# Optimization experiments

Measured on AMD Instinct MI355X. Metric: run time of the kernel, lower is better.

## Reference

```python
import jax, jax.numpy as jnp
import numpy as np

NQ, NC, D = 100000, 2000, 128
QN, CN, MAXC = 4, 4, 4
B, S = 128, 64
HOPS, RANK_K = 2, 10


def setup_inputs() -> dict:
    key = jax.random.key(0)
    ks = jax.random.split(key, 24)
    sc = 1.0 / np.sqrt(D)
    f = lambda k, shape: (jax.random.normal(k, shape) * sc).astype(jnp.float32)
    xb = float(np.sqrt(6.0 / (B + D)))  # xavier_uniform on [B, D]
    return {
        'embed_question': f(ks[0], (NQ, D)),
        'embed_concept': f(ks[1], (NC, D)),
        'embed_correctness': f(ks[2], (2, D)),
        'W_ih1': f(ks[3], (3 * D, 2 * D)), 'W_hh1': f(ks[4], (3 * D, D)),
        'b_ih1': jnp.zeros(3 * D), 'b_hh1': jnp.zeros(3 * D),
        'W_ih2': f(ks[5], (3 * D, D)), 'W_hh2': f(ks[6], (3 * D, D)),
        'b_ih2': jnp.zeros(3 * D), 'b_hh2': jnp.zeros(3 * D),
        'W_agg': f(ks[7], (HOPS, D, D)), 'b_agg': jnp.zeros((HOPS, D)),
        'W_last': f(ks[8], (D, D)), 'b_last': jnp.zeros(D),
        'W_query': f(ks[9], (D, D)), 'b_query': jnp.zeros(D),
        'W_key': f(ks[10], (D, D)), 'b_key': jnp.zeros(D),
        'w_q': f(ks[11], (D,)), 'w_k': f(ks[12], (D,)), 'b_w': jnp.zeros(()),
        'h1_init': jax.random.uniform(ks[13], (B, D), minval=-xb, maxval=xb),
        'h2_init': jax.random.uniform(ks[14], (B, D), minval=-xb, maxval=xb),
        'question_neighbors': jax.random.randint(ks[15], (NQ, QN), 0, NC),
        'concept_neighbors': jax.random.randint(ks[16], (NC, CN), 0, NQ),
        'q2c': jax.random.randint(ks[17], (NQ, MAXC), 0, NC),
        'question_seq': jax.random.randint(ks[18], (B, S), 0, NQ),
        'correctness_seq': jax.random.randint(ks[19], (B, S), 0, 2),
        'mask_seq': jax.random.randint(ks[20], (B, S), 0, 2),
    }


def _gru(x, h, Wih, Whh, bih, bhh):
    gi = x @ Wih.T + bih
    gh = h @ Whh.T + bhh
    ir, iz, inn = jnp.split(gi, 3, axis=-1)
    hr, hz, hn = jnp.split(gh, 3, axis=-1)
    r = jax.nn.sigmoid(ir + hr)
    z = jax.nn.sigmoid(iz + hz)
    n = jnp.tanh(inn + r * hn)
    return (1.0 - z) * n + z * h


def _aggregate(embs, W_agg, b_agg, W_last, b_last):
    embs = list(embs)
    for i in range(HOPS):
        for j in range(HOPS - i):
            m = jnp.mean(embs[j + 1], axis=-2) + embs[j]
            embs[j] = jnp.tanh(m @ W_agg[j].T + b_agg[j])
    return jnp.tanh(embs[0] @ W_last.T + b_last)


def _predict(qc, states, W_query, b_query, W_key, b_key, w_q, w_k, b_w):
    # qc: [B, nqc, D]; states: [B, nst, D]
    og = jnp.einsum('bqd,bsd->bqs', qc, states)
    Qe = jnp.tanh(qc @ W_key.T + b_key)          # MLP_key(question_concepts)
    Ke = jnp.tanh(states @ W_query.T + b_query)  # MLP_query(states)
    tmp = (Qe @ w_q)[:, :, None] + (Ke @ w_k)[:, None, :] + b_w  # [B,nqc,nst]
    alpha = jax.nn.softmax(tmp, axis=2)
    return jax.nn.sigmoid(jnp.sum(alpha * og, axis=(1, 2)))


def reference(embed_question, embed_concept, embed_correctness,
              W_ih1, W_hh1, b_ih1, b_hh1, W_ih2, W_hh2, b_ih2, b_hh2,
              W_agg, b_agg, W_last, b_last, W_query, b_query, W_key, b_key,
              w_q, w_k, b_w, h1_init, h2_init,
              question_neighbors, concept_neighbors, q2c,
              question_seq, correctness_seq, mask_seq):
    h1, h2 = h1_init, h2_init
    state_history = jnp.zeros((B, S, D), jnp.float32)
    y = jnp.zeros((B, S), jnp.float32)
    for t in range(S - 1):
        q_t = question_seq[:, t]
        mask_t = mask_seq[:, t] != 0
        emb_r = embed_correctness[correctness_seq[:, t]]
        # multi-hop neighbor expansion (computed for full batch; masked rows
        # are replaced below, identical math to the original masked gather)
        nodes = [q_t]
        for i in range(HOPS):
            flat = nodes[-1].reshape(-1)
            tbl = question_neighbors if i % 2 == 0 else concept_neighbors
            nxt = tbl[flat]
            nodes.append(nxt.reshape(nodes[-1].shape + (nxt.shape[-1],)))
        embs = [embed_question[n] if i % 2 == 0 else embed_concept[n]
                for i, n in enumerate(nodes)]
        agg = _aggregate(embs, W_agg, b_agg, W_last, b_last)
        emb_q = jnp.where(mask_t[:, None], agg, embed_question[q_t])
        h1 = _gru(jnp.concatenate([emb_q, emb_r], axis=1), h1, W_ih1, W_hh1, b_ih1, b_hh1)
        g2 = _gru(h1, h2, W_ih2, W_hh2, b_ih2, b_hh2)
        q_next = question_seq[:, t + 1]
        qc = jnp.concatenate([embed_question[q_next][:, None],
                              embed_concept[q2c[q_next]]], axis=1)  # [B, 1+MAXC, D]
        if t == 0:
            y = y.at[:, 0].set(_predict(qc, g2[:, None], W_query, b_query, W_key, b_key, w_q, w_k, b_w))
            continue  # original skips h2/state_history update at t==0
        cur = g2[:, None]
        if t <= RANK_K:
            hist = jnp.concatenate([cur, state_history[:, :t]], axis=1)
        else:
            Qv = jax.lax.stop_gradient(embed_question[q_next])               # [B,D]
            Kv = jax.lax.stop_gradient(embed_question[question_seq[:, :t]])  # [B,t,D]
            scores = jnp.einsum('btd,bd->bt', Kv, Qv)
            _, idx = jax.lax.top_k(scores, RANK_K)
            sel = jnp.take_along_axis(state_history, idx[:, :, None], axis=1)
            hist = jnp.concatenate([cur, sel], axis=1)
        y = y.at[:, t + 1].set(_predict(qc, hist, W_query, b_query, W_key, b_key, w_q, w_k, b_w))
        h2 = g2
        state_history = state_history.at[:, t].set(g2)
    return y
```

## Files before the change

kernel.cpp:

```cpp
#include <hip/hip_runtime.h>
#include <math.h>

#define D    128
#define QN   4
#define CN   4
#define MAXC 4
#define BB   128
#define SS   64
#define RK   10
#define T    768

#define UOFF_IH1A 0
#define UOFF_IH1B 24576
#define UOFF_HH1  49152
#define UOFF_IH2  73728
#define UOFF_HH2  98304
#define UOFF_QRY  122880
#define UOFF_A0   131072
#define UOFF_A1   139264
#define UOFF_LS   147456
#define TOTAL_U   155648

typedef _Float16 h2_t __attribute__((ext_vector_type(2)));
union U32H2 { unsigned u; h2_t h; unsigned short s2[2]; };

__device__ __forceinline__ unsigned h16f(float x){
  U32H2 c; c.h[0] = (_Float16)x; c.h[1] = (_Float16)0.f;
  return (unsigned)c.s2[0];
}
__device__ __forceinline__ unsigned packh2(float a, float b){
  U32H2 c; c.h[0] = (_Float16)a; c.h[1] = (_Float16)b;
  return c.u;
}
__device__ __forceinline__ float dot2(unsigned w, unsigned x, float acc){
  U32H2 a; a.u = w; U32H2 b; b.u = x;
  return __builtin_amdgcn_fdot2(a.h, b.h, acc, false);
}
__device__ __forceinline__ float hlo(unsigned u){ U32H2 a; a.u=u; return (float)a.h[0]; }
__device__ __forceinline__ float hhi(unsigned u){ U32H2 a; a.u=u; return (float)a.h[1]; }

__device__ __forceinline__ float fsig(float x){ return 1.f/(1.f + __expf(-x)); }
__device__ __forceinline__ float ftanh(float x){
  float xc = fminf(fmaxf(x, -30.f), 30.f);
  float e = __expf(2.f*xc);
  return (e - 1.f)/(e + 1.f);
}

#define FD4(w4, x4, acc) { \
  acc = dot2((w4).x, (x4).x, acc); acc = dot2((w4).y, (x4).y, acc); \
  acc = dot2((w4).z, (x4).z, acc); acc = dot2((w4).w, (x4).w, acc); }

__global__ void gikt_pack(const float* __restrict__ Wih1,
                          const float* __restrict__ Whh1,
                          const float* __restrict__ Wih2,
                          const float* __restrict__ Whh2,
                          const float* __restrict__ Wagg,
                          const float* __restrict__ Wlast,
                          const float* __restrict__ Wqry,
                          unsigned* __restrict__ wsU)
{
  int i = blockIdx.x * blockDim.x + threadIdx.x;
  if (i >= TOTAL_U) return;
  const float* src = nullptr; int row = 0, e2 = 0, stride = 0;
  int j = i;
  if (j < 24576) {
    int c = j & 3, i4 = j >> 2, k = i4 / 768, t = i4 - k * 768, r = t >> 1, hf = t & 1;
    e2 = hf * 32 + k * 4 + c; row = r; src = Wih1; stride = 256;
  } else if ((j -= 24576) < 24576) {
    e2 = 64 + (j / 384); row = j % 384; src = Wih1; stride = 256;
  } else if ((j -= 24576) < 24576) {
    int c = j & 3, i4 = j >> 2, k = i4 / 768, t = i4 - k * 768, r = t >> 1, hf = t & 1;
    e2 = hf * 32 + k * 4 + c; row = r; src = Whh1; stride = 128;
  } else if ((j -= 24576) < 24576) {
    int c = j & 3, i4 = j >> 2, k = i4 / 768, t = i4 - k * 768, r = t >> 1, hf = t & 1;
    e2 = hf * 32 + k * 4 + c; row = r; src = Wih2; stride = 128;
  } else if ((j -= 24576) < 24576) {
    int c = j & 3, i4 = j >> 2, k = i4 / 768, t = i4 - k * 768, r = t >> 1, hf = t & 1;
    e2 = hf * 32 + k * 4 + c; row = r; src = Whh2; stride = 128;
  } else if ((j -= 24576) < 8192) {
    int c = j & 3, i4 = j >> 2, k = i4 >> 7, r = i4 & 127;
    e2 = k * 4 + c; row = r; src = Wqry; stride = 128;
  } else if ((j -= 8192) < 8192) {
    int r = j & 127, p = (j >> 7) & 1, e2g = j >> 8;
    e2 = 2 * e2g + p; row = r; src = Wagg; stride = 128;
  } else if ((j -= 8192) < 8192) {
    int r = j & 127, p = (j >> 7) & 1, e2g = j >> 8;
    e2 = 2 * e2g + p; row = r; src = Wagg + 128 * 128; stride = 128;
  } else {
    j -= 8192;
    int r = j & 127, p = (j >> 7) & 1, e2g = j >> 8;
    e2 = 2 * e2g + p; row = r; src = Wlast; stride = 128;
  }
  float lo = src[row * stride + 2 * e2];
  float hi = src[row * stride + 2 * e2 + 1];
  wsU[i] = h16f(lo) | (h16f(hi) << 16);
}

__device__ __forceinline__ float2 gru_nl2(float2 gr, float2 gz, float2 gn,
                                          float2 hr, float2 hz, float2 hn,
                                          float2 hold){
  float2 out;
  {
    float rg = fsig(gr.x + hr.x);
    float zg = fsig(gz.x + hz.x);
    float ng = ftanh(gn.x + rg*hn.x);
    out.x = (1.f-zg)*ng + zg*hold.x;
  }
  {
    float rg = fsig(gr.y + hr.y);
    float zg = fsig(gz.y + hz.y);
    float ng = ftanh(gn.y + rg*hn.y);
    out.y = (1.f-zg)*ng + zg*hold.y;
  }
  return out;
}

__launch_bounds__(T, 1)
__global__ void gikt_main(
    const float* __restrict__ embQ,
    const float* __restrict__ embC,
    const float* __restrict__ embR,
    const float* __restrict__ b_ih1,
    const float* __restrict__ b_hh1,
    const float* __restrict__ b_ih2,
    const float* __restrict__ b_hh2,
    const float* __restrict__ b_agg,
    const float* __restrict__ b_last,
    const float* __restrict__ b_query,
    const float* __restrict__ w_k,
    const float* __restrict__ h1i,
    const float* __restrict__ h2i,
    const int* __restrict__ qnbr,
    const int* __restrict__ cnbr,
    const int* __restrict__ q2c,
    const int* __restrict__ qseq,
    const int* __restrict__ cseq,
    const int* __restrict__ mseq,
    const unsigned* __restrict__ wsU,
    float* __restrict__ y)
{
  const int b   = blockIdx.x;
  const int tid = threadIdx.x;
  const int r2  = tid >> 1, hf = tid & 1;

  __shared__ unsigned aggL[3 * 8192];
  __shared__ __align__(16) float hist[SS][132];
  __shared__ float gicorr[2][384];
  __shared__ int   idxk[SS][RK];
  __shared__ float kwh[SS];
  __shared__ __align__(16) float a_[5][D];
  __shared__ __align__(16) float gi1[3*D];
  __shared__ __align__(16) float gh1[3*D];
  __shared__ __align__(16) float gi2[3*D];
  __shared__ __align__(16) float gh2[3*D];
  __shared__ __align__(16) float h1fp[2][D];
  __shared__ __align__(16) float g2fp[2][D];
  __shared__ __align__(16) float h2ifp[D];
  __shared__ float e0[D];
  __shared__ __align__(16) float qcs[2][D];
  __shared__ float kevec[D];
  __shared__ __align__(16) unsigned mPu[5][64];
  __shared__ __align__(16) unsigned vPu[64];
  __shared__ __align__(16) unsigned m1Pu[64];
  __shared__ __align__(16) unsigned xvPu[64];
  __shared__ __align__(16) unsigned h1Pu[64];
  __shared__ __align__(16) unsigned g2Pu[64];
  __shared__ __align__(16) unsigned h2iPu[64];
  __shared__ int   sq[SS], scc[SS], smk[SS];
  __shared__ int   nn1[SS][QN], nn2[SS][QN*CN], cc2[SS][MAXC];
  __shared__ float red[12];
  __shared__ float ogv[16], kwv[16];

  float (*G)[65] = (float(*)[65])aggL;

  uint4 pw1i[8], pw1h[8], pwi[8], pwh[8];
  {
    const uint4* Pa = (const uint4*)(wsU + UOFF_IH1A);
    const uint4* Pb = (const uint4*)(wsU + UOFF_HH1);
    const uint4* Pi = (const uint4*)(wsU + UOFF_IH2);
    const uint4* Ph = (const uint4*)(wsU + UOFF_HH2);
    #pragma unroll
    for (int k = 0; k < 8; ++k) {
      pw1i[k] = Pa[k*768 + tid]; pw1h[k] = Pb[k*768 + tid];
      pwi[k]  = Pi[k*768 + tid]; pwh[k]  = Ph[k*768 + tid];
    }
  }

  for (int i = tid; i < SS; i += T) { sq[i]=qseq[b*SS+i]; scc[i]=cseq[b*SS+i]; smk[i]=mseq[b*SS+i]; }
  __syncthreads();

  for (int i = tid; i < SS*32; i += T) {
    int s = i >> 5, e4 = i & 31;
    float4 v = ((const float4*)(embQ + sq[s]*D))[e4];
    ((float4*)hist[s])[e4] = v;
  }
  for (int i = tid; i < (SS-1)*QN; i += T)   { int t = i>>2, j = i&3; nn1[t][j] = qnbr[sq[t]*QN + j]; }
  for (int i = tid; i < (SS-1)*MAXC; i += T) { int t = i>>2, j = i&3; cc2[t][j] = q2c[sq[t+1]*MAXC + j]; }
  __syncthreads();

  for (int p = tid; p < SS*SS; p += T) {
    int tq = p >> 6, s = p & 63;
    if (tq >= RK+2 && s < tq-1) {
      const float4* ra = (const float4*)hist[tq];
      const float4* rb = (const float4*)hist[s];
      float acc = 0.f;
      #pragma unroll 8
      for (int d4 = 0; d4 < 32; ++d4) {
        float4 xa = ra[d4], xb = rb[d4];
        acc += xa.x*xb.x + xa.y*xb.y + xa.z*xb.z + xa.w*xb.w;
      }
      G[tq-(RK+2)][s] = acc;
    }
  }
  for (int i = tid; i < (SS-1)*QN*CN; i += T) {
    int t = i>>4, j = (i>>2)&3, l = i&3;
    nn2[t][j*CN+l] = cnbr[nn1[t][j]*CN + l];
  }
  {
    const int c = (tid >= 384) ? 1 : 0, r = tid - (c ? 384 : 0);
    const float2* er2 = (const float2*)(embR + c*D);
    float acc = 0.f;
    #pragma unroll 4
    for (int e2l = 0; e2l < 64; ++e2l) {
      unsigned u = wsU[UOFF_IH1B + e2l*384 + r];
      float2 x = er2[e2l];
      acc += hlo(u)*x.x + hhi(u)*x.y;
    }
    gicorr[c][r] = acc;
  }
  __syncthreads();

  if (tid < 52) {
    int t = RK + 1 + tid;
    for (int k = 0; k < RK; ++k) {
      float best = -INFINITY; int bi = 0;
      for (int s = 0; s < t; ++s) { float v = G[tid][s]; if (v > best) { best = v; bi = s; } }
      idxk[t][k] = bi;
      G[tid][bi] = -INFINITY;
    }
  }
  __syncthreads();

  for (int i = tid; i < 3*8192; i += T) aggL[i] = wsU[UOFF_A0 + i];
  if (tid < 64) {
    float a0 = h1i[b*D+2*tid], a1 = h1i[b*D+2*tid+1];
    h1Pu[tid] = packh2(a0, a1);
    ((float2*)h1fp[1])[tid] = make_float2(a0, a1);
    float c0 = h2i[b*D+2*tid], c1 = h2i[b*D+2*tid+1];
    h2iPu[tid] = packh2(c0, c1);
    ((float2*)h2ifp)[tid] = make_float2(c0, c1);
    g2Pu[tid] = 0;
  }
  if (tid < D) hist[0][tid] = 0.f;
  if (tid == 0) y[b*SS + 1] = 0.f;
  {
    float p0 = (tid < D) ? w_k[tid]*ftanh(b_query[tid]) : 0.f;
    #pragma unroll
    for (int off = 32; off; off >>= 1) p0 += __shfl_down(p0, off);
    if ((tid & 63) == 0) red[tid >> 6] = p0;
  }
  __syncthreads();
  if (tid == 0) kwh[0] = red[0]+red[1];
  __syncthreads();

  const uint4* Wq4 = (const uint4*)(wsU + UOFF_QRY);

  for (int t = 0; t < SS-1; ++t) {
    const int tp = t - 1;
    const bool msk = (smk[t] != 0);

    if (tid < 64 && t >= 1) {
      const int l = tid;
      const float* ph2 = (t <= 2) ? h2ifp : g2fp[t & 1];
      float2 hold = ((const float2*)ph2)[l];
      float2 gv = gru_nl2(((const float2*)gi2)[l], ((const float2*)(gi2+128))[l], ((const float2*)(gi2+256))[l],
                          ((const float2*)gh2)[l], ((const float2*)(gh2+128))[l], ((const float2*)(gh2+256))[l],
                          hold);
      ((float2*)g2fp[(t+1)&1])[l] = gv;
      g2Pu[l] = packh2(gv.x, gv.y);
      if (t >= 2) { hist[t-1][2*l] = gv.x; hist[t-1][2*l+1] = gv.y; }
    }
    if (msk) {
      const int d   = tid & 127;
      const int grp = tid >> 7;
      if (grp == 0) {
        float ev = embQ[sq[t]*D + d];
        float s1 = embC[nn1[t][0]*D+d]+embC[nn1[t][1]*D+d]+embC[nn1[t][2]*D+d]+embC[nn1[t][3]*D+d];
        ((_Float16*)mPu[0])[d] = (_Float16)(ev + 0.25f*s1);
      } else if (grp <= 4) {
        const int j = grp - 1;
        float e1v = embC[nn1[t][j]*D + d];
        float s2  = embQ[nn2[t][j*CN+0]*D+d]+embQ[nn2[t][j*CN+1]*D+d]
                   +embQ[nn2[t][j*CN+2]*D+d]+embQ[nn2[t][j*CN+3]*D+d];
        ((_Float16*)mPu[grp])[d] = (_Float16)(e1v + 0.25f*s2);
      } else {
        float acc = embQ[sq[t+1]*D + d];
        #pragma unroll
        for (int mm = 0; mm < MAXC; ++mm) acc += embC[cc2[t][mm]*D + d];
        qcs[t & 1][d] = acc;
      }
    } else {
      const int d   = tid & 127;
      const int grp = tid >> 7;
      if (grp == 0) {
        ((_Float16*)xvPu)[d] = (_Float16)(embQ[sq[t]*D + d]);
      } else if (grp == 5) {
        float acc = embQ[sq[t+1]*D + d];
        #pragma unroll
        for (int mm = 0; mm < MAXC; ++mm) acc += embC[cc2[t][mm]*D + d];
        qcs[t & 1][d] = acc;
      }
    }
    __syncthreads();

    if (msk) {
      if (tid < 128) {
        const int r = tid;
        const unsigned* A = aggL;
        const uint2* x2p = (const uint2*)mPu[0];
        float acc0 = b_agg[r], acc1 = 0.f;
        #pragma unroll
        for (int e2g = 0; e2g < 32; e2g += 2) {
          unsigned u00 = A[e2g*256 + r],     u01 = A[e2g*256 + 128 + r];
          uint2 x0 = x2p[e2g];
          acc0 = dot2(u00, x0.x, acc0); acc0 = dot2(u01, x0.y, acc0);
          unsigned u10 = A[(e2g+1)*256 + r], u11 = A[(e2g+1)*256 + 128 + r];
          uint2 x1 = x2p[e2g+1];
          acc1 = dot2(u10, x1.x, acc1); acc1 = dot2(u11, x1.y, acc1);
        }
        a_[0][r] = ftanh(acc0 + acc1);
      } else if (tid < 256) {
        const int r = tid - 128;
        const unsigned* A = aggL + 8192;
        const uint2* x1p = (const uint2*)mPu[1];
        const uint2* x2p = (const uint2*)mPu[2];
        const uint2* x3p = (const uint2*)mPu[3];
        const uint2* x4p = (const uint2*)mPu[4];
        float bb = b_agg[D + r];
        float c1 = 0.f, c2 = 0.f, c3 = 0.f, c4 = 0.f;
        #pragma unroll
        for (int e2g = 0; e2g < 32; ++e2g) {
          unsigned u0 = A[e2g*256 + r], u1 = A[e2g*256 + 128 + r];
          uint2 v1 = x1p[e2g]; c1 = dot2(u0, v1.x, c1); c1 = dot2(u1, v1.y, c1);
          uint2 v2 = x2p[e2g]; c2 = dot2(u0, v2.x, c2); c2 = dot2(u1, v2.y, c2);
          uint2 v3 = x3p[e2g]; c3 = dot2(u0, v3.x, c3); c3 = dot2(u1, v3.y, c3);
          uint2 v4 = x4p[e2g]; c4 = dot2(u0, v4.x, c4); c4 = dot2(u1, v4.y, c4);
        }
        a_[1][r] = ftanh(bb + c1); a_[2][r] = ftanh(bb + c2);
        a_[3][r] = ftanh(bb + c3); a_[4][r] = ftanh(bb + c4);
      } else if (tid < 432 && t >= 1) {
        const int g = (tid - 256) >> 4, lane = tid & 15;
        const int ne = (tp < RK ? tp : RK) + 1;
        if (g < ne) {
          const float* row;
          if (g == 0) row = g2fp[(t+1)&1];
          else {
            int s = (tp <= RK) ? (g-1) : idxk[tp][g-1];
            row = hist[s];
            if (lane == 0) kwv[g] = kwh[s];
          }
          const float* qp = qcs[tp & 1];
          float part = 0.f;
          #pragma unroll
          for (int k = 0; k < 8; ++k) { int d = lane + (k<<4); part += qp[d]*row[d]; }
          part += __shfl_xor(part, 8, 16);
          part += __shfl_xor(part, 4, 16);
          part += __shfl_xor(part, 2, 16);
          part += __shfl_xor(part, 1, 16);
          if (lane == 0) ogv[g] = part;
        }
      } else if (tid >= 512) {
        const int rq = (tid - 512) >> 1, hq = tid & 1;
        const uint4* g2p4 = (const uint4*)g2Pu;
        float a0 = hq ? 0.f : b_query[rq], a1 = 0.f;
        #pragma unroll
        for (int k = hq*8; k < hq*8+8; k += 2) {
          uint4 u0 = Wq4[k*128 + rq];     uint4 x0 = g2p4[k];   FD4(u0, x0, a0);
          uint4 u1 = Wq4[(k+1)*128 + rq]; uint4 x1 = g2p4[k+1]; FD4(u1, x1, a1);
        }
        float acc = a0 + a1; acc += __shfl_xor(acc, 1);
        if (!hq) kevec[rq] = ftanh(acc) * w_k[rq];
      }
      __syncthreads();

      if (tid < 256) {
        const int l = tid & 63;
        float v0 = a_[0][2*l]   + 0.25f*(a_[1][2*l]  +a_[2][2*l]  +a_[3][2*l]  +a_[4][2*l]);
        float v1 = a_[0][2*l+1] + 0.25f*(a_[1][2*l+1]+a_[2][2*l+1]+a_[3][2*l+1]+a_[4][2*l+1]);
        vPu[l] = packh2(v0, v1);
        const int r = tid >> 1, h = tid & 1;
        const uint2* x2p = (const uint2*)vPu;
        float acc0 = h ? 0.f : b_agg[r], acc1 = 0.f;
        #pragma unroll
        for (int e2g = h*16; e2g < h*16+16; e2g += 2) {
          unsigned u00 = aggL[e2g*256 + r],     u01 = aggL[e2g*256 + 128 + r];
          uint2 x0 = x2p[e2g];
          acc0 = dot2(u00, x0.x, acc0); acc0 = dot2(u01, x0.y, acc0);
          unsigned u10 = aggL[(e2g+1)*256 + r], u11 = aggL[(e2g+1)*256 + 128 + r];
          uint2 x1 = x2p[e2g+1];
          acc1 = dot2(u10, x1.x, acc1); acc1 = dot2(u11, x1.y, acc1);
        }
        float acc = acc0 + acc1; acc += __shfl_xor(acc, 1);
        if (!h) ((_Float16*)m1Pu)[r] = (_Float16)ftanh(acc);
      } else if (tid >= 512 && tid < 576 && t >= 1) {
        const int lane = tid & 63;
        float v = kevec[lane] + kevec[lane + 64];
        #pragma unroll
        for (int off = 32; off; off >>= 1) v += __shfl_down(v, off);
        if (lane == 0) { kwv[0] = v; if (tp >= 1) kwh[tp] = v; }
      }
      __syncthreads();

      if (tid < 256) {
        const int r = tid >> 1, h = tid & 1;
        const unsigned* A = aggL + 16384;
        const uint2* x2p = (const uint2*)m1Pu;
        float acc0 = h ? 0.f : b_last[r], acc1 = 0.f;
        #pragma unroll
        for (int e2g = h*16; e2g < h*16+16; e2g += 2) {
          unsigned u00 = A[e2g*256 + r],     u01 = A[e2g*256 + 128 + r];
          uint2 x0 = x2p[e2g];
          acc0 = dot2(u00, x0.x, acc0); acc0 = dot2(u01, x0.y, acc0);
          unsigned u10 = A[(e2g+1)*256 + r], u11 = A[(e2g+1)*256 + 128 + r];
          uint2 x1 = x2p[e2g+1];
          acc1 = dot2(u10, x1.x, acc1); acc1 = dot2(u11, x1.y, acc1);
        }
        float acc = acc0 + acc1; acc += __shfl_xor(acc, 1);
        if (!h) ((_Float16*)xvPu)[r] = (_Float16)ftanh(acc);
      } else if (tid == 256 && t >= 1) {
        const int ne = (tp < RK ? tp : RK) + 1;
        float mx = kwv[0];
        for (int i2 = 1; i2 < ne; ++i2) mx = fmaxf(mx, kwv[i2]);
        float den = 0.f, num = 0.f;
        for (int i2 = 0; i2 < ne; ++i2) { float e_ = __expf(kwv[i2]-mx); den += e_; num += e_*ogv[i2]; }
        y[b*SS + ((tp==0) ? 0 : (tp+1))] = fsig(num/den);
      }
      __syncthreads();

      {
        const uint4* xvp4 = (const uint4*)xvPu;
        const uint4* h1p4 = (const uint4*)h1Pu;
        float ai0 = hf ? 0.f : (b_ih1[r2] + gicorr[scc[t]][r2]), ai1 = 0.f;
        float ah0 = hf ? 0.f : b_hh1[r2], ah1 = 0.f;
        #pragma unroll
        for (int k = 0; k < 8; k += 2) {
          uint4 xa = xvp4[hf*8+k], xb = xvp4[hf*8+k+1];
          FD4(pw1i[k], xa, ai0); FD4(pw1i[k+1], xb, ai1);
          uint4 ya = h1p4[hf*8+k], yb = h1p4[hf*8+k+1];
          FD4(pw1h[k], ya, ah0); FD4(pw1h[k+1], yb, ah1);
        }
        float acc_i = ai0 + ai1; acc_i += __shfl_xor(acc_i, 1);
        float acc_h = ah0 + ah1; acc_h += __shfl_xor(acc_h, 1);
        if (!hf) { gi1[r2] = acc_i; gh1[r2] = acc_h; }
      }
      __syncthreads();
    } else {
      if (tid >= 256 && tid < 432 && t >= 1) {
        const int g = (tid - 256) >> 4, lane = tid & 15;
        const int ne = (tp < RK ? tp : RK) + 1;
        if (g < ne) {
          const float* row;
          if (g == 0) row = g2fp[(t+1)&1];
          else {
            int s = (tp <= RK) ? (g-1) : idxk[tp][g-1];
            row = hist[s];
            if (lane == 0) kwv[g] = kwh[s];
          }
          const float* qp = qcs[tp & 1];
          float part = 0.f;
          #pragma unroll
          for (int k = 0; k < 8; ++k) { int d = lane + (k<<4); part += qp[d]*row[d]; }
          part += __shfl_xor(part, 8, 16);
          part += __shfl_xor(part, 4, 16);
          part += __shfl_xor(part, 2, 16);
          part += __shfl_xor(part, 1, 16);
          if (lane == 0) ogv[g] = part;
        }
      } else if (tid >= 512) {
        const int rq = (tid - 512) >> 1, hq = tid & 1;
        const uint4* g2p4 = (const uint4*)g2Pu;
        float a0 = hq ? 0.f : b_query[rq], a1 = 0.f;
        #pragma unroll
        for (int k = hq*8; k < hq*8+8; k += 2) {
          uint4 u0 = Wq4[k*128 + rq];     uint4 x0 = g2p4[k];   FD4(u0, x0, a0);
          uint4 u1 = Wq4[(k+1)*128 + rq]; uint4 x1 = g2p4[k+1]; FD4(u1, x1, a1);
        }
        float acc = a0 + a1; acc += __shfl_xor(acc, 1);
        if (!hq) kevec[rq] = ftanh(acc) * w_k[rq];
      }
      {
        const uint4* xvp4 = (const uint4*)xvPu;
        const uint4* h1p4 = (const uint4*)h1Pu;
        float ai0 = hf ? 0.f : (b_ih1[r2] + gicorr[scc[t]][r2]), ai1 = 0.f;
        float ah0 = hf ? 0.f : b_hh1[r2], ah1 = 0.f;
        #pragma unroll
        for (int k = 0; k < 8; k += 2) {
          uint4 xa = xvp4[hf*8+k], xb = xvp4[hf*8+k+1];
          FD4(pw1i[k], xa, ai0); FD4(pw1i[k+1], xb, ai1);
          uint4 ya = h1p4[hf*8+k], yb = h1p4[hf*8+k+1];
          FD4(pw1h[k], ya, ah0); FD4(pw1h[k+1], yb, ah1);
        }
        float acc_i = ai0 + ai1; acc_i += __shfl_xor(acc_i, 1);
        float acc_h = ah0 + ah1; acc_h += __shfl_xor(acc_h, 1);
        if (!hf) { gi1[r2] = acc_i; gh1[r2] = acc_h; }
      }
      __syncthreads();
    }

    if (!msk && t >= 1 && tid < 64) {
      float v = kevec[tid] + kevec[tid + 64];
      #pragma unroll
      for (int off = 32; off; off >>= 1) v += __shfl_down(v, off);
      if (tid == 0) {
        if (tp >= 1) kwh[tp] = v;
        const int ne = (tp < RK ? tp : RK) + 1;
        float mx = v;
        for (int i2 = 1; i2 < ne; ++i2) mx = fmaxf(mx, kwv[i2]);
        float den = __expf(v - mx), num = den*ogv[0];
        for (int i2 = 1; i2 < ne; ++i2) { float e_ = __expf(kwv[i2]-mx); den += e_; num += e_*ogv[i2]; }
        y[b*SS + ((tp==0) ? 0 : (tp+1))] = fsig(num/den);
      }
    }
    {
      const int l = tid & 63;
      float2 hold = ((const float2*)h1fp[(t+1)&1])[l];
      float2 hn = gru_nl2(((const float2*)gi1)[l], ((const float2*)(gi1+128))[l], ((const float2*)(gi1+256))[l],
                          ((const float2*)gh1)[l], ((const float2*)(gh1+128))[l], ((const float2*)(gh1+256))[l],
                          hold);
      ((float2*)h1fp[t&1])[l] = hn;
      h1Pu[l] = packh2(hn.x, hn.y);
    }
    {
      const uint4* xh1 = (const uint4*)h1Pu;
      const uint4* xh2 = (t <= 1) ? (const uint4*)h2iPu : (const uint4*)g2Pu;
      float ai0 = hf ? 0.f : b_ih2[r2], ai1 = 0.f;
      float ah0 = hf ? 0.f : b_hh2[r2], ah1 = 0.f;
      #pragma unroll
      for (int k = 0; k < 8; k += 2) {
        uint4 xa = xh1[hf*8+k], xb = xh1[hf*8+k+1];
        FD4(pwi[k], xa, ai0); FD4(pwi[k+1], xb, ai1);
        uint4 ya = xh2[hf*8+k], yb = xh2[hf*8+k+1];
        FD4(pwh[k], ya, ah0); FD4(pwh[k+1], yb, ah1);
      }
      float acc_i = ai0 + ai1; acc_i += __shfl_xor(acc_i, 1);
      float acc_h = ah0 + ah1; acc_h += __shfl_xor(acc_h, 1);
      if (!hf) { gi2[r2] = acc_i; gh2[r2] = acc_h; }
    }
    __syncthreads();
  }

  if (tid < 64) {
    const int l = tid;
    const float* ph2 = g2fp[1];
    float2 hold = ((const float2*)ph2)[l];
    float2 gv = gru_nl2(((const float2*)gi2)[l], ((const float2*)(gi2+128))[l], ((const float2*)(gi2+256))[l],
                        ((const float2*)gh2)[l], ((const float2*)(gh2+128))[l], ((const float2*)(gh2+256))[l],
                        hold);
    ((float2*)g2fp[0])[l] = gv;
    g2Pu[l] = packh2(gv.x, gv.y);
  }
  __syncthreads();
  if (tid < 128) {
    const int r = tid;
    const uint4* g2p4 = (const uint4*)g2Pu;
    float a0 = b_query[r], a1 = 0.f;
    #pragma unroll
    for (int k = 0; k < 16; k += 2) {
      uint4 u0 = Wq4[k*128 + r];     uint4 x0 = g2p4[k];   FD4(u0, x0, a0);
      uint4 u1 = Wq4[(k+1)*128 + r]; uint4 x1 = g2p4[k+1]; FD4(u1, x1, a1);
    }
    kevec[r] = ftanh(a0 + a1) * w_k[r];
  }
  __syncthreads();
  {
    const int tp = SS - 2;
    if (tid < 176) {
      const int g = tid >> 4, lane = tid & 15;
      const int ne = RK + 1;
      if (g < ne) {
        const float* row;
        if (g == 0) row = g2fp[0];
        else {
          int s = idxk[tp][g-1];
          row = hist[s];
          if (lane == 0) kwv[g] = kwh[s];
        }
        const float* qp = qcs[tp & 1];
        float part = 0.f;
        #pragma unroll
        for (int k = 0; k < 8; ++k) { int d = lane + (k<<4); part += qp[d]*row[d]; }
        part += __shfl_xor(part, 8, 16);
        part += __shfl_xor(part, 4, 16);
        part += __shfl_xor(part, 2, 16);
        part += __shfl_xor(part, 1, 16);
        if (lane == 0) ogv[g] = part;
      }
    } else if (tid >= 256 && tid < 320) {
      const int lane = tid & 63;
      float v = kevec[lane] + kevec[lane + 64];
      #pragma unroll
      for (int off = 32; off; off >>= 1) v += __shfl_down(v, off);
      if (lane == 0) kwv[0] = v;
    }
  }
  __syncthreads();
  if (tid == 0) {
    const int ne = RK + 1;
    float mx = kwv[0];
    for (int i2 = 1; i2 < ne; ++i2) mx = fmaxf(mx, kwv[i2]);
    float den = 0.f, num = 0.f;
    for (int i2 = 0; i2 < ne; ++i2) { float e_ = __expf(kwv[i2]-mx); den += e_; num += e_*ogv[i2]; }
    y[b*SS + SS - 1] = fsig(num/den);
  }
}

extern "C" void kernel_launch(void* const* d_in, const int* in_sizes, int n_in,
                              void* d_out, int out_size, void* d_ws, size_t ws_size,
                              hipStream_t stream)
{
  (void)in_sizes; (void)n_in; (void)out_size; (void)ws_size;

  const float* embQ  = (const float*)d_in[0];
  const float* embC  = (const float*)d_in[1];
  const float* embR  = (const float*)d_in[2];
  const float* Wih1  = (const float*)d_in[3];
  const float* Whh1  = (const float*)d_in[4];
  const float* bih1  = (const float*)d_in[5];
  const float* bhh1  = (const float*)d_in[6];
  const float* Wih2  = (const float*)d_in[7];
  const float* Whh2  = (const float*)d_in[8];
  const float* bih2  = (const float*)d_in[9];
  const float* bhh2  = (const float*)d_in[10];
  const float* Wagg  = (const float*)d_in[11];
  const float* bagg  = (const float*)d_in[12];
  const float* Wlast = (const float*)d_in[13];
  const float* blast = (const float*)d_in[14];
  const float* Wqry  = (const float*)d_in[15];
  const float* bqry  = (const float*)d_in[16];
  const float* wk    = (const float*)d_in[20];
  const float* h1i   = (const float*)d_in[22];
  const float* h2i   = (const float*)d_in[23];
  const int* qnbr    = (const int*)d_in[24];
  const int* cnbr    = (const int*)d_in[25];
  const int* q2c     = (const int*)d_in[26];
  const int* qseq    = (const int*)d_in[27];
  const int* cseq    = (const int*)d_in[28];
  const int* mseq    = (const int*)d_in[29];

  unsigned* wsU = (unsigned*)d_ws;
  float* yout = (float*)d_out;

  gikt_pack<<<(TOTAL_U + 255) / 256, 256, 0, stream>>>(Wih1, Whh1, Wih2, Whh2, Wagg, Wlast, Wqry, wsU);
  gikt_main<<<BB, T, 0, stream>>>(embQ, embC, embR, bih1, bhh1, bih2, bhh2, bagg, blast, bqry,
                                  wk, h1i, h2i, qnbr, cnbr, q2c, qseq, cseq, mseq, wsU, yout);
}
```

Before: 640.4 us.

## Prefetch next-step embedding gathers into registers and stream GRU1 weights from memory

The embedding and neighbour gathers for step t+1 are now issued into registers during step t, so their global-memory latency overlaps the barrier and the compute phases instead of sitting on the serial critical path. To make room for these registers, the layer-1 GRU weights are no longer held in registers; they are reloaded from the packed global buffer (likely L2-resident) on every step. An empty asm keeps the layer-2 weights pinned in registers. The trade-off is more per-step weight load traffic and latency in the GRU1 matvec in exchange for hidden gather latency and lower register pressure.

```diff
diff --git a/kernel.cpp b/kernel.cpp
--- a/kernel.cpp
+++ b/kernel.cpp
@@ -49,6 +49,8 @@
 #define FD4(w4, x4, acc) { \
   acc = dot2((w4).x, (x4).x, acc); acc = dot2((w4).y, (x4).y, acc); \
   acc = dot2((w4).z, (x4).z, acc); acc = dot2((w4).w, (x4).w, acc); }
+
+#define KEEP4(v) asm volatile("" : "+v"((v).x), "+v"((v).y), "+v"((v).z), "+v"((v).w))
 
 __global__ void gikt_pack(const float* __restrict__ Wih1,
                           const float* __restrict__ Whh1,
@@ -156,7 +158,6 @@
   __shared__ __align__(16) float h1fp[2][D];
   __shared__ __align__(16) float g2fp[2][D];
   __shared__ __align__(16) float h2ifp[D];
-  __shared__ float e0[D];
   __shared__ __align__(16) float qcs[2][D];
   __shared__ float kevec[D];
   __shared__ __align__(16) unsigned mPu[5][64];
@@ -173,17 +174,14 @@
 
   float (*G)[65] = (float(*)[65])aggL;
 
-  uint4 pw1i[8], pw1h[8], pwi[8], pwh[8];
+  uint4 pwi[8], pwh[8];
   {
-    const uint4* Pa = (const uint4*)(wsU + UOFF_IH1A);
-    const uint4* Pb = (const uint4*)(wsU + UOFF_HH1);
     const uint4* Pi = (const uint4*)(wsU + UOFF_IH2);
     const uint4* Ph = (const uint4*)(wsU + UOFF_HH2);
     #pragma unroll
-    for (int k = 0; k < 8; ++k) {
-      pw1i[k] = Pa[k*768 + tid]; pw1h[k] = Pb[k*768 + tid];
-      pwi[k]  = Pi[k*768 + tid]; pwh[k]  = Ph[k*768 + tid];
-    }
+    for (int k = 0; k < 8; ++k) { pwi[k] = Pi[k*768 + tid]; pwh[k] = Ph[k*768 + tid]; }
+    #pragma unroll
+    for (int k = 0; k < 8; ++k) { KEEP4(pwi[k]); KEEP4(pwh[k]); }
   }
 
   for (int i = tid; i < SS; i += T) { sq[i]=qseq[b*SS+i]; scc[i]=cseq[b*SS+i]; smk[i]=mseq[b*SS+i]; }
@@ -263,7 +261,31 @@
   if (tid == 0) kwh[0] = red[0]+red[1];
   __syncthreads();
 
+  const uint4* Wi1 = (const uint4*)(wsU + UOFF_IH1A);
+  const uint4* Wh1 = (const uint4*)(wsU + UOFF_HH1);
   const uint4* Wq4 = (const uint4*)(wsU + UOFF_QRY);
+
+  float pf0 = 0.f, pf1 = 0.f, pf2 = 0.f, pf3 = 0.f, pf4 = 0.f;
+
+#define PREFETCH(tt) {                                                        \
+    const int d_ = tid & 127, grp_ = tid >> 7;                                \
+    const bool m2_ = (smk[tt] != 0);                                          \
+    if (grp_ == 0) {                                                          \
+      pf0 = embQ[sq[tt]*D + d_];                                              \
+      if (m2_) { pf1 = embC[nn1[tt][0]*D+d_]; pf2 = embC[nn1[tt][1]*D+d_];    \
+                 pf3 = embC[nn1[tt][2]*D+d_]; pf4 = embC[nn1[tt][3]*D+d_]; }  \
+    } else if (grp_ <= 4) {                                                   \
+      if (m2_) { const int j_ = grp_ - 1;                                     \
+        pf0 = embC[nn1[tt][j_]*D + d_];                                       \
+        pf1 = embQ[nn2[tt][j_*CN+0]*D+d_]; pf2 = embQ[nn2[tt][j_*CN+1]*D+d_]; \
+        pf3 = embQ[nn2[tt][j_*CN+2]*D+d_]; pf4 = embQ[nn2[tt][j_*CN+3]*D+d_];}\
+    } else {                                                                  \
+      pf0 = embQ[sq[(tt)+1]*D + d_];                                          \
+      pf1 = embC[cc2[tt][0]*D+d_]; pf2 = embC[cc2[tt][1]*D+d_];               \
+      pf3 = embC[cc2[tt][2]*D+d_]; pf4 = embC[cc2[tt][3]*D+d_];               \
+    } }
+
+  PREFETCH(0);
 
   for (int t = 0; t < SS-1; ++t) {
     const int tp = t - 1;
@@ -280,37 +302,17 @@
       g2Pu[l] = packh2(gv.x, gv.y);
       if (t >= 2) { hist[t-1][2*l] = gv.x; hist[t-1][2*l+1] = gv.y; }
     }
-    if (msk) {
-      const int d   = tid & 127;
-      const int grp = tid >> 7;
-      if (grp == 0) {
-        float ev = embQ[sq[t]*D + d];
-        float s1 = embC[nn1[t][0]*D+d]+embC[nn1[t][1]*D+d]+embC[nn1[t][2]*D+d]+embC[nn1[t][3]*D+d];
-        ((_Float16*)mPu[0])[d] = (_Float16)(ev + 0.25f*s1);
-      } else if (grp <= 4) {
-        const int j = grp - 1;
-        float e1v = embC[nn1[t][j]*D + d];
-        float s2  = embQ[nn2[t][j*CN+0]*D+d]+embQ[nn2[t][j*CN+1]*D+d]
-                   +embQ[nn2[t][j*CN+2]*D+d]+embQ[nn2[t][j*CN+3]*D+d];
-        ((_Float16*)mPu[grp])[d] = (_Float16)(e1v + 0.25f*s2);
+    {
+      const int d = tid & 127, grp = tid >> 7;
+      if (msk) {
+        if (grp <= 4) ((_Float16*)mPu[grp])[d] = (_Float16)(pf0 + 0.25f*(pf1+pf2+pf3+pf4));
+        else          qcs[t & 1][d] = pf0+pf1+pf2+pf3+pf4;
       } else {
-        float acc = embQ[sq[t+1]*D + d];
-        #pragma unroll
-        for (int mm = 0; mm < MAXC; ++mm) acc += embC[cc2[t][mm]*D + d];
-        qcs[t & 1][d] = acc;
-      }
-    } else {
-      const int d   = tid & 127;
-      const int grp = tid >> 7;
-      if (grp == 0) {
-        ((_Float16*)xvPu)[d] = (_Float16)(embQ[sq[t]*D + d]);
-      } else if (grp == 5) {
-        float acc = embQ[sq[t+1]*D + d];
-        #pragma unroll
-        for (int mm = 0; mm < MAXC; ++mm) acc += embC[cc2[t][mm]*D + d];
-        qcs[t & 1][d] = acc;
-      }
-    }
+        if (grp == 0)      ((_Float16*)xvPu)[d] = (_Float16)pf0;
+        else if (grp == 5) qcs[t & 1][d] = pf0+pf1+pf2+pf3+pf4;
+      }
+    }
+    if (t + 1 < SS-1) PREFETCH(t+1);
     __syncthreads();
 
     if (msk) {
@@ -444,10 +446,12 @@
         float ah0 = hf ? 0.f : b_hh1[r2], ah1 = 0.f;
         #pragma unroll
         for (int k = 0; k < 8; k += 2) {
+          uint4 w0 = Wi1[k*768 + tid], w1 = Wi1[(k+1)*768 + tid];
           uint4 xa = xvp4[hf*8+k], xb = xvp4[hf*8+k+1];
-          FD4(pw1i[k], xa, ai0); FD4(pw1i[k+1], xb, ai1);
+          FD4(w0, xa, ai0); FD4(w1, xb, ai1);
+          uint4 v0 = Wh1[k*768 + tid], v1 = Wh1[(k+1)*768 + tid];
           uint4 ya = h1p4[hf*8+k], yb = h1p4[hf*8+k+1];
-          FD4(pw1h[k], ya, ah0); FD4(pw1h[k+1], yb, ah1);
+          FD4(v0, ya, ah0); FD4(v1, yb, ah1);
         }
         float acc_i = ai0 + ai1; acc_i += __shfl_xor(acc_i, 1);
         float acc_h = ah0 + ah1; acc_h += __shfl_xor(acc_h, 1);
@@ -495,10 +499,12 @@
         float ah0 = hf ? 0.f : b_hh1[r2], ah1 = 0.f;
         #pragma unroll
         for (int k = 0; k < 8; k += 2) {
+          uint4 w0 = Wi1[k*768 + tid], w1 = Wi1[(k+1)*768 + tid];
           uint4 xa = xvp4[hf*8+k], xb = xvp4[hf*8+k+1];
-          FD4(pw1i[k], xa, ai0); FD4(pw1i[k+1], xb, ai1);
+          FD4(w0, xa, ai0); FD4(w1, xb, ai1);
+          uint4 v0 = Wh1[k*768 + tid], v1 = Wh1[(k+1)*768 + tid];
           uint4 ya = h1p4[hf*8+k], yb = h1p4[hf*8+k+1];
-          FD4(pw1h[k], ya, ah0); FD4(pw1h[k+1], yb, ah1);
+          FD4(v0, ya, ah0); FD4(v1, yb, ah1);
         }
         float acc_i = ai0 + ai1; acc_i += __shfl_xor(acc_i, 1);
         float acc_h = ah0 + ah1; acc_h += __shfl_xor(acc_h, 1);
```

Result: faster. 546.2 us (-14.7%).
